# Kernel tuning notes

Hardware: AMD Instinct MI355X
Metric: run time of the kernel (lower is better)

The kernel has to match this reference:

```python
import jax, jax.numpy as jnp
import numpy as np

BS, L, D, N = 4, 2048, 1024, 16

def setup_inputs() -> dict:
    key = jax.random.key(0)
    ks = jax.random.split(key, 8)
    s = 1.0 / np.sqrt(D)
    x  = jax.random.normal(ks[0], (BS, L, D), dtype=jnp.float32)
    # torch Linear params; stored transposed so y = x @ W + b
    W1 = jax.random.uniform(ks[1], (D, D), jnp.float32, -s, s)
    b1 = jax.random.uniform(ks[2], (D,),   jnp.float32, -s, s)
    W2 = jax.random.uniform(ks[3], (D, N), jnp.float32, -s, s)
    b2 = jax.random.uniform(ks[4], (N,),   jnp.float32, -s, s)
    W3 = jax.random.uniform(ks[5], (D, N), jnp.float32, -s, s)
    b3 = jax.random.uniform(ks[6], (N,),   jnp.float32, -s, s)
    A  = jax.random.normal(ks[7], (D, N),  jnp.float32) * np.sqrt(2.0 / (D + N))  # xavier
    return {"x": x, "W1": W1, "b1": b1, "W2": W2, "b2": b2, "W3": W3, "b3": b3, "A": A}

def reference(x, W1, b1, W2, b2, W3, b3, A):
    # S6 forward (non-recurrent branch).
    B = x @ W2 + b2                     # (b,l,n)
    C = x @ W3 + b3                     # (b,l,n)
    delta = jax.nn.softplus(x @ W1 + b1)  # (b,l,d)
    # dA = exp(einsum('bld,dn->bldn', delta, A)) is multiplied by an all-zero h
    # in the original forward, so it does not affect the output (dead code under DCE).
    dB = jnp.einsum('bld,bln->bldn', delta, B)   # (b,l,d,n) -- 512 MB intermediate
    h = x[..., None] * dB                         # (b,l,d,n)
    y = jnp.einsum('bln,bldn->bld', C, h)         # (b,l,d)
    return y
```

## Files before the change

kernel.cpp:

```cpp
#include <hip/hip_runtime.h>
#include <hip/hip_bf16.h>
#include <math.h>


#define GLB(p) ((const __attribute__((address_space(1))) void*)(p))
#define LDSP(p) ((__attribute__((address_space(3))) void*)(p))

namespace {

constexpr int Dd   = 1024;
constexpr int ROWS = 8192;

typedef __bf16 bf16x8 __attribute__((ext_vector_type(8)));
typedef float  floatx4 __attribute__((ext_vector_type(4)));

__device__ __forceinline__ float softplus_fast(float v) {
    float l = __logf(1.0f + __expf(v));
    return v > 15.0f ? v : l;
}
__device__ __forceinline__ float bf_lo(unsigned short u) {
    union { unsigned q; float f; } c; c.q = ((unsigned)u) << 16; return c.f;
}

__global__ __launch_bounds__(256) void w23_kernel(
    const float* __restrict__ W2, const float* __restrict__ W3,
    __bf16* __restrict__ W2t, __bf16* __restrict__ W3t)
{
    const int t  = threadIdx.x;
    const int n  = t >> 4;
    const int kc = (t & 15) * 64;
    #pragma unroll
    for (int i8 = 0; i8 < 8; ++i8) {
        bf16x8 a, b;
        #pragma unroll
        for (int j = 0; j < 8; ++j) {
            const int k = kc + i8 * 8 + j;
            a[j] = (__bf16)W2[(size_t)k * 16 + n];
            b[j] = (__bf16)W3[(size_t)k * 16 + n];
        }
        *(bf16x8*)&W2t[(size_t)n * Dd + kc + i8 * 8] = a;
        *(bf16x8*)&W3t[(size_t)n * Dd + kc + i8 * 8] = b;
    }
}

__global__ __launch_bounds__(256, 4) void prep_kernel(
    const float* __restrict__ X, const float* __restrict__ W1,
    const __bf16* __restrict__ W2t, const float* __restrict__ b2,
    const __bf16* __restrict__ W3t, const float* __restrict__ b3,
    __bf16* __restrict__ Xb, __bf16* __restrict__ W1t, float* __restrict__ Sv)
{
    const int t = threadIdx.x;

    if (blockIdx.x >= 512) {
        __shared__ __bf16 tile[64][66];
        const int bidx = blockIdx.x - 512;
        const int bi = bidx >> 4, bj = bidx & 15;
        const int c = t & 63, r4 = t >> 6;
        #pragma unroll
        for (int i = 0; i < 16; ++i) {
            const int r = i * 4 + r4;
            tile[r][c] = (__bf16)W1[(size_t)(bi * 64 + r) * Dd + bj * 64 + c];
        }
        __syncthreads();
        #pragma unroll
        for (int i = 0; i < 16; ++i) {
            const int r = i * 4 + r4;
            W1t[(size_t)(bj * 64 + r) * Dd + bi * 64 + c] = tile[c][r];
        }
        return;
    }

    __shared__ float red[4][2][16][16];
    __shared__ float pbuf[16][16];
    const int w = t >> 6, lane = t & 63;
    const int l15 = lane & 15, quad = lane >> 4;
    const int row0 = blockIdx.x * 16;
    const int kw = w * 256;
    const size_t xoff = (size_t)(row0 + l15) * Dd;
    const size_t woff = (size_t)l15 * Dd;

    floatx4 acc0 = {0.f, 0.f, 0.f, 0.f}, acc1 = {0.f, 0.f, 0.f, 0.f};
    #pragma unroll
    for (int ks = 0; ks < 8; ++ks) {
        const int k0 = kw + ks * 32 + quad * 8;
        const float4 xa = *(const float4*)&X[xoff + k0];
        const float4 xb = *(const float4*)&X[xoff + k0 + 4];
        bf16x8 af;
        af[0] = (__bf16)xa.x; af[1] = (__bf16)xa.y;
        af[2] = (__bf16)xa.z; af[3] = (__bf16)xa.w;
        af[4] = (__bf16)xb.x; af[5] = (__bf16)xb.y;
        af[6] = (__bf16)xb.z; af[7] = (__bf16)xb.w;
        *(bf16x8*)&Xb[xoff + k0] = af;
        const bf16x8 w2f = *(const bf16x8*)&W2t[woff + k0];
        const bf16x8 w3f = *(const bf16x8*)&W3t[woff + k0];
        acc0 = __builtin_amdgcn_mfma_f32_16x16x32_bf16(af, w2f, acc0, 0, 0, 0);
        acc1 = __builtin_amdgcn_mfma_f32_16x16x32_bf16(af, w3f, acc1, 0, 0, 0);
    }
    #pragma unroll
    for (int r = 0; r < 4; ++r) {
        red[w][0][quad * 4 + r][l15] = acc0[r];
        red[w][1][quad * 4 + r][l15] = acc1[r];
    }
    __syncthreads();
    {
        const int r = t & 15, n = t >> 4;
        if (n < 16) {
            float B = b2[n], C = b3[n];
            #pragma unroll
            for (int ww = 0; ww < 4; ++ww) {
                B += red[ww][0][r][n];
                C += red[ww][1][r][n];
            }
            pbuf[r][n] = B * C;
        }
    }
    __syncthreads();
    if (t < 16) {
        float s = 0.f;
        #pragma unroll
        for (int n = 0; n < 16; ++n) s += pbuf[t][n];
        Sv[row0 + t] = s;
    }
}

__global__ __launch_bounds__(256, 2) void gemm_kernel(
    const __bf16* __restrict__ Xb, const __bf16* __restrict__ W1t,
    const float* __restrict__ Sv, const float* __restrict__ b1,
    float* __restrict__ Y)
{
    __shared__ __attribute__((aligned(16))) __bf16 lds[16384];
    const int t = threadIdx.x, lane = t & 63;
    const int w = t >> 6, wm = w & 1, wn = w >> 1;
    const int l15 = lane & 15, quad = lane >> 4;
    const int cb = blockIdx.x & 7, rb = blockIdx.x >> 3;
    const int row0 = rb * 128, col0 = cb * 128;

    floatx4 acc[4][4] = {};

    const __bf16* gA[4]; const __bf16* gB[4];
    int dA[4], dB[4];
    #pragma unroll
    for (int r = 0; r < 4; ++r) {
        const int u = r * 256 + t;
        const int p = u >> 3, s = u & 7, c4 = s ^ (p & 7);
        gA[r] = Xb  + (size_t)(row0 + p) * Dd + c4 * 8;
        gB[r] = W1t + (size_t)(col0 + p) * Dd + c4 * 8;
        dA[r] = u * 8;
        dB[r] = 8192 + u * 8;
    }

    const int arl[4] = { wm * 64 + 0 * 16 + l15, wm * 64 + 1 * 16 + l15,
                         wm * 64 + 2 * 16 + l15, wm * 64 + 3 * 16 + l15 };
    const int brl[4] = { wn * 64 + 0 * 16 + l15, wn * 64 + 1 * 16 + l15,
                         wn * 64 + 2 * 16 + l15, wn * 64 + 3 * 16 + l15 };

    for (int k0 = 0; k0 < Dd; k0 += 64) {
        #pragma unroll
        for (int r = 0; r < 4; ++r) {
            __builtin_amdgcn_global_load_lds(GLB(gA[r] + k0), LDSP(&lds[dA[r]]), 16, 0, 0);
            __builtin_amdgcn_global_load_lds(GLB(gB[r] + k0), LDSP(&lds[dB[r]]), 16, 0, 0);
        }
        __syncthreads();

        #pragma unroll
        for (int ksub = 0; ksub < 2; ++ksub) {
            bf16x8 af[4], bfr[4];
            #pragma unroll
            for (int mt = 0; mt < 4; ++mt) {
                const int rl = arl[mt];
                const int sA = (ksub * 4 + quad) ^ (rl & 7);
                af[mt] = *(const bf16x8*)&lds[rl * 64 + sA * 8];
            }
            #pragma unroll
            for (int nt = 0; nt < 4; ++nt) {
                const int nl = brl[nt];
                const int sB = (ksub * 4 + quad) ^ (nl & 7);
                bfr[nt] = *(const bf16x8*)&lds[8192 + nl * 64 + sB * 8];
            }
            #pragma unroll
            for (int mt = 0; mt < 4; ++mt)
                #pragma unroll
                for (int nt = 0; nt < 4; ++nt)
                    acc[mt][nt] = __builtin_amdgcn_mfma_f32_16x16x32_bf16(
                        af[mt], bfr[nt], acc[mt][nt], 0, 0, 0);
        }
        __syncthreads();
    }

    float bias[4];
    #pragma unroll
    for (int nt = 0; nt < 4; ++nt) bias[nt] = b1[col0 + wn * 64 + nt * 16 + l15];

    #pragma unroll
    for (int mt = 0; mt < 4; ++mt) {
        #pragma unroll
        for (int rr = 0; rr < 4; ++rr) {
            const int row = row0 + wm * 64 + mt * 16 + quad * 4 + rr;
            const float sv = Sv[row];
            const unsigned short* xrow =
                (const unsigned short*)(Xb + (size_t)row * Dd + col0);
            float* yrow = Y + (size_t)row * Dd + col0;
            #pragma unroll
            for (int nt = 0; nt < 4; ++nt) {
                const int cl = wn * 64 + nt * 16 + l15;
                const float v  = acc[mt][nt][rr] + bias[nt];
                const float sp = softplus_fast(v);
                yrow[cl] = bf_lo(xrow[cl]) * sp * sv;
            }
        }
    }
}

}

extern "C" void kernel_launch(void* const* d_in, const int* in_sizes, int n_in,
                              void* d_out, int out_size, void* d_ws, size_t ws_size,
                              hipStream_t stream)
{
    const float* X  = (const float*)d_in[0];
    const float* W1 = (const float*)d_in[1];
    const float* b1 = (const float*)d_in[2];
    const float* W2 = (const float*)d_in[3];
    const float* b2 = (const float*)d_in[4];
    const float* W3 = (const float*)d_in[5];
    const float* b3 = (const float*)d_in[6];
    float* Y = (float*)d_out;

    char* ws = (char*)d_ws;
    __bf16* Xb  = (__bf16*)ws;
    __bf16* W1t = (__bf16*)(ws + 16777216);
    float*  Sv  = (float*) (ws + 16777216 + 2097152);
    __bf16* W2t = (__bf16*)(ws + 16777216 + 2097152 + 32768);
    __bf16* W3t = (__bf16*)(ws + 16777216 + 2097152 + 65536);

    hipLaunchKernelGGL(w23_kernel, dim3(1), dim3(256), 0, stream, W2, W3, W2t, W3t);
    hipLaunchKernelGGL(prep_kernel, dim3(768), dim3(256), 0, stream,
                       X, W1, W2t, b2, W3t, b3, Xb, W1t, Sv);
    hipLaunchKernelGGL(gemm_kernel, dim3((ROWS / 128) * (Dd / 128)), dim3(256), 0, stream,
                       Xb, W1t, Sv, b1, Y);
}
```

Before: 147.6 us.

## Register-prefetch GEMM with half-size LDS, parallelize W2/W3 transpose, shuffle-reduce Sv

The GEMM main loop switches from direct global-to-LDS loads of a 64-wide K slab to register-staged loads of 32-wide K slabs. The next slab is prefetched into registers while the current one is computed, and the LDS footprint is halved, which may allow higher occupancy. The W2/W3 transpose kernel now runs on 16 blocks instead of one, and the prep kernel's final row reduction uses warp shuffles in place of an extra LDS buffer and barrier. The GEMM loop now needs four barriers per 64-K step and holds more prefetch registers.

```diff
diff --git a/kernel.cpp b/kernel.cpp
--- a/kernel.cpp
+++ b/kernel.cpp
@@ -3,9 +3,6 @@
 #include <math.h>
 
 
-#define GLB(p) ((const __attribute__((address_space(1))) void*)(p))
-#define LDSP(p) ((__attribute__((address_space(3))) void*)(p))
-
 namespace {
 
 constexpr int Dd   = 1024;
@@ -13,6 +10,8 @@
 
 typedef __bf16 bf16x8 __attribute__((ext_vector_type(8)));
 typedef float  floatx4 __attribute__((ext_vector_type(4)));
+
+#define LDS_BAR() asm volatile("s_waitcnt lgkmcnt(0)\n\ts_barrier" ::: "memory")
 
 __device__ __forceinline__ float softplus_fast(float v) {
     float l = __logf(1.0f + __expf(v));
@@ -28,19 +27,19 @@
 {
     const int t  = threadIdx.x;
     const int n  = t >> 4;
-    const int kc = (t & 15) * 64;
-    #pragma unroll
-    for (int i8 = 0; i8 < 8; ++i8) {
-        bf16x8 a, b;
-        #pragma unroll
-        for (int j = 0; j < 8; ++j) {
-            const int k = kc + i8 * 8 + j;
-            a[j] = (__bf16)W2[(size_t)k * 16 + n];
-            b[j] = (__bf16)W3[(size_t)k * 16 + n];
-        }
-        *(bf16x8*)&W2t[(size_t)n * Dd + kc + i8 * 8] = a;
-        *(bf16x8*)&W3t[(size_t)n * Dd + kc + i8 * 8] = b;
-    }
+    const int k0 = blockIdx.x * 64 + (t & 15) * 4;
+    ushort4 a, b;
+    union { __bf16 h; unsigned short u; } c;
+    c.h = (__bf16)W2[(size_t)(k0 + 0) * 16 + n]; a.x = c.u;
+    c.h = (__bf16)W2[(size_t)(k0 + 1) * 16 + n]; a.y = c.u;
+    c.h = (__bf16)W2[(size_t)(k0 + 2) * 16 + n]; a.z = c.u;
+    c.h = (__bf16)W2[(size_t)(k0 + 3) * 16 + n]; a.w = c.u;
+    c.h = (__bf16)W3[(size_t)(k0 + 0) * 16 + n]; b.x = c.u;
+    c.h = (__bf16)W3[(size_t)(k0 + 1) * 16 + n]; b.y = c.u;
+    c.h = (__bf16)W3[(size_t)(k0 + 2) * 16 + n]; b.z = c.u;
+    c.h = (__bf16)W3[(size_t)(k0 + 3) * 16 + n]; b.w = c.u;
+    *(ushort4*)&W2t[(size_t)n * Dd + k0] = a;
+    *(ushort4*)&W3t[(size_t)n * Dd + k0] = b;
 }
 
 __global__ __launch_bounds__(256, 4) void prep_kernel(
@@ -71,7 +70,6 @@
     }
 
     __shared__ float red[4][2][16][16];
-    __shared__ float pbuf[16][16];
     const int w = t >> 6, lane = t & 63;
     const int l15 = lane & 15, quad = lane >> 4;
     const int row0 = blockIdx.x * 16;
@@ -103,23 +101,17 @@
     }
     __syncthreads();
     {
-        const int r = t & 15, n = t >> 4;
-        if (n < 16) {
-            float B = b2[n], C = b3[n];
-            #pragma unroll
-            for (int ww = 0; ww < 4; ++ww) {
-                B += red[ww][0][r][n];
-                C += red[ww][1][r][n];
-            }
-            pbuf[r][n] = B * C;
-        }
-    }
-    __syncthreads();
-    if (t < 16) {
-        float s = 0.f;
-        #pragma unroll
-        for (int n = 0; n < 16; ++n) s += pbuf[t][n];
-        Sv[row0 + t] = s;
+        const int r = t >> 4, n = t & 15;
+        float B = b2[n], C = b3[n];
+        #pragma unroll
+        for (int ww = 0; ww < 4; ++ww) {
+            B += red[ww][0][r][n];
+            C += red[ww][1][r][n];
+        }
+        float p = B * C;
+        p += __shfl_xor(p, 1); p += __shfl_xor(p, 2);
+        p += __shfl_xor(p, 4); p += __shfl_xor(p, 8);
+        if (n == 0) Sv[row0 + r] = p;
     }
 }
 
@@ -128,7 +120,7 @@
     const float* __restrict__ Sv, const float* __restrict__ b1,
     float* __restrict__ Y)
 {
-    __shared__ __attribute__((aligned(16))) __bf16 lds[16384];
+    __shared__ __attribute__((aligned(16))) __bf16 lds[8192];
     const int t = threadIdx.x, lane = t & 63;
     const int w = t >> 6, wm = w & 1, wn = w >> 1;
     const int l15 = lane & 15, quad = lane >> 4;
@@ -137,54 +129,69 @@
 
     floatx4 acc[4][4] = {};
 
-    const __bf16* gA[4]; const __bf16* gB[4];
-    int dA[4], dB[4];
-    #pragma unroll
-    for (int r = 0; r < 4; ++r) {
+    const __bf16* gA[2]; const __bf16* gB[2];
+    int dA[2], dB[2];
+    #pragma unroll
+    for (int r = 0; r < 2; ++r) {
         const int u = r * 256 + t;
         const int p = u >> 3, s = u & 7, c4 = s ^ (p & 7);
-        gA[r] = Xb  + (size_t)(row0 + p) * Dd + c4 * 8;
-        gB[r] = W1t + (size_t)(col0 + p) * Dd + c4 * 8;
+        const int rowL = 2 * p + (c4 >> 2), chk = c4 & 3;
+        gA[r] = Xb  + (size_t)(row0 + rowL) * Dd + chk * 8;
+        gB[r] = W1t + (size_t)(col0 + rowL) * Dd + chk * 8;
         dA[r] = u * 8;
-        dB[r] = 8192 + u * 8;
-    }
-
-    const int arl[4] = { wm * 64 + 0 * 16 + l15, wm * 64 + 1 * 16 + l15,
-                         wm * 64 + 2 * 16 + l15, wm * 64 + 3 * 16 + l15 };
-    const int brl[4] = { wn * 64 + 0 * 16 + l15, wn * 64 + 1 * 16 + l15,
-                         wn * 64 + 2 * 16 + l15, wn * 64 + 3 * 16 + l15 };
-
+        dB[r] = 4096 + u * 8;
+    }
+
+    bf16x8 bufA[2][2], bufB[2][2];
+
+    auto gload = [&](int buf, int k) {
+        #pragma unroll
+        for (int r = 0; r < 2; ++r) {
+            bufA[buf][r] = *(const bf16x8*)(gA[r] + k);
+            bufB[buf][r] = *(const bf16x8*)(gB[r] + k);
+        }
+    };
+    auto store_lds = [&](int buf) {
+        #pragma unroll
+        for (int r = 0; r < 2; ++r) {
+            *(bf16x8*)&lds[dA[r]] = bufA[buf][r];
+            *(bf16x8*)&lds[dB[r]] = bufB[buf][r];
+        }
+    };
+    auto compute = [&]() {
+        bf16x8 af[4], bfr[4];
+        #pragma unroll
+        for (int mt = 0; mt < 4; ++mt) {
+            const int rl = wm * 64 + mt * 16 + l15;
+            const int p = rl >> 1, c4 = ((rl & 1) << 2) | quad, s = c4 ^ (p & 7);
+            af[mt] = *(const bf16x8*)&lds[p * 64 + s * 8];
+        }
+        #pragma unroll
+        for (int nt = 0; nt < 4; ++nt) {
+            const int nl = wn * 64 + nt * 16 + l15;
+            const int p = nl >> 1, c4 = ((nl & 1) << 2) | quad, s = c4 ^ (p & 7);
+            bfr[nt] = *(const bf16x8*)&lds[4096 + p * 64 + s * 8];
+        }
+        #pragma unroll
+        for (int mt = 0; mt < 4; ++mt)
+            #pragma unroll
+            for (int nt = 0; nt < 4; ++nt)
+                acc[mt][nt] = __builtin_amdgcn_mfma_f32_16x16x32_bf16(
+                    af[mt], bfr[nt], acc[mt][nt], 0, 0, 0);
+    };
+
+    gload(0, 0);
     for (int k0 = 0; k0 < Dd; k0 += 64) {
-        #pragma unroll
-        for (int r = 0; r < 4; ++r) {
-            __builtin_amdgcn_global_load_lds(GLB(gA[r] + k0), LDSP(&lds[dA[r]]), 16, 0, 0);
-            __builtin_amdgcn_global_load_lds(GLB(gB[r] + k0), LDSP(&lds[dB[r]]), 16, 0, 0);
-        }
-        __syncthreads();
-
-        #pragma unroll
-        for (int ksub = 0; ksub < 2; ++ksub) {
-            bf16x8 af[4], bfr[4];
-            #pragma unroll
-            for (int mt = 0; mt < 4; ++mt) {
-                const int rl = arl[mt];
-                const int sA = (ksub * 4 + quad) ^ (rl & 7);
-                af[mt] = *(const bf16x8*)&lds[rl * 64 + sA * 8];
-            }
-            #pragma unroll
-            for (int nt = 0; nt < 4; ++nt) {
-                const int nl = brl[nt];
-                const int sB = (ksub * 4 + quad) ^ (nl & 7);
-                bfr[nt] = *(const bf16x8*)&lds[8192 + nl * 64 + sB * 8];
-            }
-            #pragma unroll
-            for (int mt = 0; mt < 4; ++mt)
-                #pragma unroll
-                for (int nt = 0; nt < 4; ++nt)
-                    acc[mt][nt] = __builtin_amdgcn_mfma_f32_16x16x32_bf16(
-                        af[mt], bfr[nt], acc[mt][nt], 0, 0, 0);
-        }
-        __syncthreads();
+        gload(1, k0 + 32);
+        LDS_BAR();
+        store_lds(0);
+        LDS_BAR();
+        compute();
+        if (k0 + 64 < Dd) gload(0, k0 + 64);
+        LDS_BAR();
+        store_lds(1);
+        LDS_BAR();
+        compute();
     }
 
     float bias[4];
@@ -233,7 +240,7 @@
     __bf16* W2t = (__bf16*)(ws + 16777216 + 2097152 + 32768);
     __bf16* W3t = (__bf16*)(ws + 16777216 + 2097152 + 65536);
 
-    hipLaunchKernelGGL(w23_kernel, dim3(1), dim3(256), 0, stream, W2, W3, W2t, W3t);
+    hipLaunchKernelGGL(w23_kernel, dim3(16), dim3(256), 0, stream, W2, W3, W2t, W3t);
     hipLaunchKernelGGL(prep_kernel, dim3(768), dim3(256), 0, stream,
                        X, W1, W2t, b2, W3t, b3, Xb, W1t, Sv);
     hipLaunchKernelGGL(gemm_kernel, dim3((ROWS / 128) * (Dd / 128)), dim3(256), 0, stream,
```

After: 135.4 us. -8.2%, faster.
